# Kernel optimization log

Hardware: AMD Instinct MI355X
Metric: run time of the kernel (lower is better)

## Reference

```python
import jax, jax.numpy as jnp
import numpy as np

B, T, D, H = 2, 2048, 1024, 16
HS = D // H  # head_size = 64
EPS = 1e-5


def layer_norm(x, g, b):
    mu = jnp.mean(x, axis=-1, keepdims=True)
    var = jnp.var(x, axis=-1, keepdims=True)
    return (x - mu) * jax.lax.rsqrt(var + EPS) * g + b


def setup_inputs() -> dict:
    key = jax.random.key(0)
    ks = jax.random.split(key, 12)
    s_attn = 1.0 / np.sqrt(D)
    s_ff1 = 1.0 / np.sqrt(D)
    s_ff2 = 1.0 / np.sqrt(4 * D)
    return {
        "x": jax.random.normal(ks[0], (B, T, D), jnp.float32),
        "Wq": jax.random.normal(ks[1], (H, D, HS), jnp.float32) * s_attn,
        "Wk": jax.random.normal(ks[2], (H, D, HS), jnp.float32) * s_attn,
        "Wv": jax.random.normal(ks[3], (H, D, HS), jnp.float32) * s_attn,
        "Wo": jax.random.normal(ks[4], (H * HS, D), jnp.float32) * (1.0 / np.sqrt(H * HS)),
        "bo": jnp.zeros((D,), jnp.float32),
        "W1": jax.random.normal(ks[5], (D, 4 * D), jnp.float32) * s_ff1,
        "b1": jnp.zeros((4 * D,), jnp.float32),
        "W2": jax.random.normal(ks[6], (4 * D, D), jnp.float32) * s_ff2,
        "b2": jnp.zeros((D,), jnp.float32),
        "ln1_g": jnp.ones((D,), jnp.float32),
        "ln1_b": jnp.zeros((D,), jnp.float32),
        "ln2_g": jnp.ones((D,), jnp.float32),
        "ln2_b": jnp.zeros((D,), jnp.float32),
    }


def reference(x, Wq, Wk, Wv, Wo, bo, W1, b1, W2, b2, ln1_g, ln1_b, ln2_g, ln2_b):
    # --- self-attention on ln1(x) ---
    h = layer_norm(x, ln1_g, ln1_b)
    Q = jnp.einsum('bsd,hdk->bhsk', h, Wq)
    K = jnp.einsum('bsd,hdk->bhsk', h, Wk)
    V = jnp.einsum('bsd,hdk->bhsk', h, Wv)
    scores = jnp.einsum('bhqk,bhsk->bhqs', Q, K) * (HS ** -0.5)
    attn = jax.nn.softmax(scores, axis=-1)  # [B,H,T,T] non-causal, as in source
    out = jnp.einsum('bhqs,bhsk->bhqk', attn, V)
    out = out.transpose(0, 2, 1, 3).reshape(B, T, H * HS)  # concat heads
    sa = out @ Wo + bo
    x = x + sa
    # --- feed-forward on ln2(x) ---
    h2 = layer_norm(x, ln2_g, ln2_b)
    ff = jax.nn.relu(h2 @ W1 + b1) @ W2 + b2
    return x + ff
```

## Files before the change

### kernel.cpp

```cpp
#include <hip/hip_runtime.h>
#include <cstdint>
#include <cmath>

typedef __bf16 bf16;
typedef __bf16 bf16x8 __attribute__((ext_vector_type(8)));
typedef __bf16 bf16x4 __attribute__((ext_vector_type(4)));
typedef __bf16 bf16x2 __attribute__((ext_vector_type(2)));
typedef float  f32x4  __attribute__((ext_vector_type(4)));

#define B_   2
#define T_   2048
#define D_   1024
#define H_   16
#define HS_  64
#define NTOK (B_ * T_)

typedef __attribute__((address_space(1))) uint8_t* gp1_t;
typedef __attribute__((address_space(3))) uint8_t* lp3_t;
__device__ __forceinline__ void gl_lds16(const void* g, void* l) {
    __builtin_amdgcn_global_load_lds((gp1_t)(uintptr_t)g,
                                     (lp3_t)(uint32_t)(uintptr_t)l,
                                     16, 0, 0);
}

__device__ __forceinline__ f32x4 mfma16(bf16x8 a, bf16x8 b, f32x4 c) {
    return __builtin_amdgcn_mfma_f32_16x16x32_bf16(a, b, c, 0, 0, 0);
}

__device__ __forceinline__ uint32_t pk2(float lo, float hi) {
    uint32_t r;
    asm("v_cvt_pk_bf16_f32 %0, %1, %2" : "=v"(r) : "v"(lo), "v"(hi));
    return r;
}
__device__ __forceinline__ void pl32(uint32_t& a, uint32_t& b) {
    asm("v_permlane32_swap_b32 %0, %1" : "+v"(a), "+v"(b));
}
__device__ __forceinline__ void pl16(uint32_t& a, uint32_t& b) {
    asm("v_permlane16_swap_b32 %0, %1" : "+v"(a), "+v"(b));
}

__global__ __launch_bounds__(256) void prep_fused(
    const float* __restrict__ Wq, const float* __restrict__ Wk,
    const float* __restrict__ Wv, const float* __restrict__ Wo,
    const float* __restrict__ W1, const float* __restrict__ W2,
    const float* __restrict__ x,  const float* __restrict__ g,
    const float* __restrict__ be,
    bf16* __restrict__ WqkvT, bf16* __restrict__ WoT,
    bf16* __restrict__ W1T,  bf16* __restrict__ W2T,
    bf16* __restrict__ hbuf) {
    const int bid = blockIdx.x;
    const int tid = threadIdx.x;

    if (bid >= 12288) {
        const int row = bid - 12288;
        const float4 v = ((const float4*)(x + (size_t)row * 1024))[tid];
        float s  = v.x + v.y + v.z + v.w;
        float s2 = v.x * v.x + v.y * v.y + v.z * v.z + v.w * v.w;
        for (int m = 1; m < 64; m <<= 1) {
            s  += __shfl_xor(s, m);
            s2 += __shfl_xor(s2, m);
        }
        __shared__ float rs[4], rq[4];
        const int lane = tid & 63, wv = tid >> 6;
        if (lane == 0) { rs[wv] = s; rq[wv] = s2; }
        __syncthreads();
        s  = rs[0] + rs[1] + rs[2] + rs[3];
        s2 = rq[0] + rq[1] + rq[2] + rq[3];
        const float mu   = s * (1.f / 1024.f);
        const float var  = s2 * (1.f / 1024.f) - mu * mu;
        const float rstd = rsqrtf(var + 1e-5f);
        const float4 gg = ((const float4*)g)[tid];
        const float4 bb = ((const float4*)be)[tid];
        bf16x4 o;
        o[0] = (bf16)((v.x - mu) * rstd * gg.x + bb.x);
        o[1] = (bf16)((v.y - mu) * rstd * gg.y + bb.y);
        o[2] = (bf16)((v.z - mu) * rstd * gg.z + bb.z);
        o[3] = (bf16)((v.w - mu) * rstd * gg.w + bb.w);
        *(bf16x4*)(hbuf + (size_t)row * 1024 + tid * 4) = o;
        return;
    }

    const float* in; bf16* out;
    int C, R, bx, by;
    if (bid < 3072) {
        const int z = bid >> 6, rem = bid & 63;
        bx = rem & 1; by = rem >> 1;
        C = HS_; R = D_;
        in  = (z < 16 ? Wq : z < 32 ? Wk : Wv) + (size_t)(z & 15) * D_ * HS_;
        out = WqkvT + (size_t)z * HS_ * D_;
    } else if (bid < 4096) {
        const int rem = bid - 3072;
        bx = rem & 31; by = rem >> 5;
        C = 1024; R = 1024; in = Wo; out = WoT;
    } else if (bid < 8192) {
        const int rem = bid - 4096;
        bx = rem & 127; by = rem >> 7;
        C = 4096; R = 1024; in = W1; out = W1T;
    } else {
        const int rem = bid - 8192;
        bx = rem & 31; by = rem >> 5;
        C = 1024; R = 4096; in = W2; out = W2T;
    }
    const int tx = tid & 31, ty = tid >> 5;
    const int c0 = bx * 32, r0 = by * 32;
    __shared__ float t[32][33];
    for (int i = 0; i < 4; i++) {
        int r = ty + i * 8;
        t[r][tx] = in[(size_t)(r0 + r) * C + c0 + tx];
    }
    __syncthreads();
    for (int i = 0; i < 4; i++) {
        int rr = ty + i * 8;
        out[(size_t)(c0 + rr) * R + r0 + tx] = (bf16)t[tx][rr];
    }
}

__global__ __launch_bounds__(256) void ln_kernel(const float* __restrict__ x,
                                                 const float* __restrict__ g,
                                                 const float* __restrict__ b,
                                                 bf16* __restrict__ out) {
    const int row = blockIdx.x;
    const int tid = threadIdx.x;
    const float4 v = ((const float4*)(x + (size_t)row * 1024))[tid];
    float s  = v.x + v.y + v.z + v.w;
    float s2 = v.x * v.x + v.y * v.y + v.z * v.z + v.w * v.w;
    for (int m = 1; m < 64; m <<= 1) {
        s  += __shfl_xor(s, m);
        s2 += __shfl_xor(s2, m);
    }
    __shared__ float rs[4], rq[4];
    const int lane = tid & 63, wv = tid >> 6;
    if (lane == 0) { rs[wv] = s; rq[wv] = s2; }
    __syncthreads();
    s  = rs[0] + rs[1] + rs[2] + rs[3];
    s2 = rq[0] + rq[1] + rq[2] + rq[3];
    const float mu   = s * (1.f / 1024.f);
    const float var  = s2 * (1.f / 1024.f) - mu * mu;
    const float rstd = rsqrtf(var + 1e-5f);
    const float4 gg = ((const float4*)g)[tid];
    const float4 bb = ((const float4*)b)[tid];
    bf16x4 o;
    o[0] = (bf16)((v.x - mu) * rstd * gg.x + bb.x);
    o[1] = (bf16)((v.y - mu) * rstd * gg.y + bb.y);
    o[2] = (bf16)((v.z - mu) * rstd * gg.z + bb.z);
    o[3] = (bf16)((v.w - mu) * rstd * gg.w + bb.w);
    *(bf16x4*)(out + (size_t)row * 1024 + tid * 4) = o;
}

__global__ __launch_bounds__(256) void combine4(const float* __restrict__ p0,
                                                const float* __restrict__ p1,
                                                const float* __restrict__ p2,
                                                const float* __restrict__ p3,
                                                const float* __restrict__ resid,
                                                const float* __restrict__ bias,
                                                float* __restrict__ out) {
    const int i4 = blockIdx.x * 256 + threadIdx.x;
    const float4 a = ((const float4*)p0)[i4];
    const float4 b = ((const float4*)p1)[i4];
    const float4 c = ((const float4*)p2)[i4];
    const float4 d = ((const float4*)p3)[i4];
    const float4 r = ((const float4*)resid)[i4];
    const float4 bb = ((const float4*)bias)[i4 & 255];
    float4 o;
    o.x = a.x + b.x + c.x + d.x + r.x + bb.x;
    o.y = a.y + b.y + c.y + d.y + r.y + bb.y;
    o.z = a.z + b.z + c.z + d.z + r.z + bb.z;
    o.w = a.w + b.w + c.w + d.w + r.w + bb.w;
    ((float4*)out)[i4] = o;
}

template <int BIAS, int RELU, int RES, int OUTBF16, int VTP = 0>
__global__ __launch_bounds__(256, 2) void gemm_bt(
    const bf16* __restrict__ A, const bf16* __restrict__ Bt,
    const float* __restrict__ bias, const float* __restrict__ resid,
    void* __restrict__ Cout, bf16* __restrict__ Vt, int M, int N, int K) {
    __shared__ __align__(16) bf16 As[2][128 * 32];
    __shared__ __align__(16) bf16 Bs[2][128 * 32];
    const int tid  = threadIdx.x;
    const int lane = tid & 63, w = tid >> 6;
    const int quad = lane >> 4, l15 = lane & 15;
    const int m0 = blockIdx.y * 128, n0 = blockIdx.x * 128;
    const int wm = (w & 1) * 64, wn = (w >> 1) * 64;

    f32x4 acc[4][4];
    for (int i = 0; i < 4; i++)
        for (int j = 0; j < 4; j++) acc[i][j] = f32x4{0.f, 0.f, 0.f, 0.f};

    const int arow = lane >> 2;
    const int acol = (lane & 3) * 8;
    const int c0 = w * 2, c1 = w * 2 + 1;

    for (int kt = 0; kt < K; kt += 64) {
        gl_lds16(A  + (size_t)(m0 + c0 * 16 + arow) * K + kt + acol,      &As[0][c0 * 512]);
        gl_lds16(A  + (size_t)(m0 + c1 * 16 + arow) * K + kt + acol,      &As[0][c1 * 512]);
        gl_lds16(A  + (size_t)(m0 + c0 * 16 + arow) * K + kt + 32 + acol, &As[1][c0 * 512]);
        gl_lds16(A  + (size_t)(m0 + c1 * 16 + arow) * K + kt + 32 + acol, &As[1][c1 * 512]);
        gl_lds16(Bt + (size_t)(n0 + c0 * 16 + arow) * K + kt + acol,      &Bs[0][c0 * 512]);
        gl_lds16(Bt + (size_t)(n0 + c1 * 16 + arow) * K + kt + acol,      &Bs[0][c1 * 512]);
        gl_lds16(Bt + (size_t)(n0 + c0 * 16 + arow) * K + kt + 32 + acol, &Bs[1][c0 * 512]);
        gl_lds16(Bt + (size_t)(n0 + c1 * 16 + arow) * K + kt + 32 + acol, &Bs[1][c1 * 512]);
        __syncthreads();
        for (int kh = 0; kh < 2; kh++) {
            bf16x8 af[4], bfr[4];
            for (int mi = 0; mi < 4; mi++)
                af[mi] = *(const bf16x8*)&As[kh][(wm + mi * 16 + l15) * 32 + quad * 8];
            for (int ni = 0; ni < 4; ni++)
                bfr[ni] = *(const bf16x8*)&Bs[kh][(wn + ni * 16 + l15) * 32 + quad * 8];
            for (int mi = 0; mi < 4; mi++)
                for (int ni = 0; ni < 4; ni++)
                    acc[mi][ni] = mfma16(af[mi], bfr[ni], acc[mi][ni]);
        }
        __syncthreads();
    }

    for (int mi = 0; mi < 4; mi++) {
        for (int ni = 0; ni < 4; ni++) {
            const int colb = n0 + wn + ni * 16 + l15;
            if (VTP && colb >= 2048) {
                const int h = (colb - 2048) >> 6, hs = (colb - 2048) & 63;
                const int row0 = m0 + wm + mi * 16 + quad * 4;
                const int b = row0 >> 11;
                bf16x4 p4;
                p4[0] = (bf16)acc[mi][ni][0];
                p4[1] = (bf16)acc[mi][ni][1];
                p4[2] = (bf16)acc[mi][ni][2];
                p4[3] = (bf16)acc[mi][ni][3];
                *(bf16x4*)&Vt[((size_t)(b * 16 + h) * 64 + hs) * T_ + (row0 & 2047)] = p4;
                continue;
            }
            const float bv = BIAS ? bias[colb] : 0.f;
            for (int r = 0; r < 4; r++) {
                const int row = m0 + wm + mi * 16 + quad * 4 + r;
                float v = acc[mi][ni][r] + bv;
                if (RELU) v = fmaxf(v, 0.f);
                if (RES)  v += resid[(size_t)row * N + colb];
                if (OUTBF16) ((bf16*)Cout)[(size_t)row * N + colb] = (bf16)v;
                else         ((float*)Cout)[(size_t)row * N + colb] = v;
            }
        }
    }
}

template <int BIAS, int RELU, int VTP, int PARTIAL>
__global__ __launch_bounds__(512, 2) void gemm256(
    const bf16* __restrict__ A, const bf16* __restrict__ Bt,
    const float* __restrict__ bias, void* __restrict__ Cout,
    bf16* __restrict__ Vt, float* __restrict__ P0, float* __restrict__ P1,
    int M, int N, int K) {
    __shared__ __align__(16) bf16 Asub[4][256 * 32];
    __shared__ __align__(16) bf16 Bsub[4][256 * 32];
    const int tid  = threadIdx.x;
    const int lane = tid & 63, w = tid >> 6;
    const int wr = w >> 2, wc = w & 3;
    const int quad = lane >> 4, l15 = lane & 15;
    const int m0 = blockIdx.y * 256, n0 = blockIdx.x * 256;
    const int kpb = PARTIAL ? (K / (int)gridDim.z) : K;
    const int k0  = PARTIAL ? (int)blockIdx.z * kpb : 0;
    const int S   = kpb / 32;

    const int slog = (((lane & 3) ^ ((lane >> 3) & 3)) * 8);
    const int crow = lane >> 2;
    const bf16* gA0 = A  + (size_t)(m0 + 32 * w + crow)      * K + k0 + slog;
    const bf16* gA1 = A  + (size_t)(m0 + 32 * w + 16 + crow) * K + k0 + slog;
    const bf16* gB0 = Bt + (size_t)(n0 + 32 * w + crow)      * K + k0 + slog;
    const bf16* gB1 = Bt + (size_t)(n0 + 32 * w + 16 + crow) * K + k0 + slog;

    for (int t = 0; t < 3; t++) {
        gl_lds16(gA0, &Asub[t][(32 * w) * 32]);
        gl_lds16(gA1, &Asub[t][(32 * w + 16) * 32]);
        gl_lds16(gB0, &Bsub[t][(32 * w) * 32]);
        gl_lds16(gB1, &Bsub[t][(32 * w + 16) * 32]);
        gA0 += 32; gA1 += 32; gB0 += 32; gB1 += 32;
    }

    f32x4 acc[8][4];
#pragma unroll
    for (int i = 0; i < 8; i++)
#pragma unroll
        for (int j = 0; j < 4; j++) acc[i][j] = f32x4{0.f, 0.f, 0.f, 0.f};

    const int swz = (quad ^ ((l15 >> 1) & 3)) * 8;
    const int aof = (wr * 128 + l15) * 32 + swz;
    const int bof = (wc * 64 + l15) * 32 + swz;

    asm volatile("s_waitcnt vmcnt(8)" ::: "memory");
    __builtin_amdgcn_sched_barrier(0);
    __builtin_amdgcn_s_barrier();

    for (int s = 0; s < S; s++) {
        const bf16* Ab = &Asub[s & 3][0];
        const bf16* Bb = &Bsub[s & 3][0];
        const int pb = (s + 3) & 3;
        bf16x8 af[4], bfr[4];
#pragma unroll
        for (int f = 0; f < 4; f++) af[f] = *(const bf16x8*)&Ab[aof + f * 512];
#pragma unroll
        for (int n = 0; n < 4; n++) bfr[n] = *(const bf16x8*)&Bb[bof + n * 512];
        if (s + 3 < S) {
            gl_lds16(gA0, &Asub[pb][(32 * w) * 32]);
            gl_lds16(gA1, &Asub[pb][(32 * w + 16) * 32]);
            gA0 += 32; gA1 += 32;
        }
        asm volatile("s_waitcnt lgkmcnt(0)" ::: "memory");
        __builtin_amdgcn_sched_barrier(0);
        __builtin_amdgcn_s_setprio(1);
#pragma unroll
        for (int f = 0; f < 4; f++)
#pragma unroll
            for (int n = 0; n < 4; n++)
                acc[f][n] = mfma16(af[f], bfr[n], acc[f][n]);
        __builtin_amdgcn_s_setprio(0);
#pragma unroll
        for (int f = 0; f < 4; f++) af[f] = *(const bf16x8*)&Ab[aof + 2048 + f * 512];
        if (s + 3 < S) {
            gl_lds16(gB0, &Bsub[pb][(32 * w) * 32]);
            gl_lds16(gB1, &Bsub[pb][(32 * w + 16) * 32]);
            gB0 += 32; gB1 += 32;
        }
        asm volatile("s_waitcnt lgkmcnt(0)" ::: "memory");
        __builtin_amdgcn_sched_barrier(0);
        __builtin_amdgcn_s_setprio(1);
#pragma unroll
        for (int f = 0; f < 4; f++)
#pragma unroll
            for (int n = 0; n < 4; n++)
                acc[4 + f][n] = mfma16(af[f], bfr[n], acc[4 + f][n]);
        __builtin_amdgcn_s_setprio(0);
        __builtin_amdgcn_sched_barrier(0);
        if (s <= S - 4)      asm volatile("s_waitcnt vmcnt(8)" ::: "memory");
        else if (s == S - 3) asm volatile("s_waitcnt vmcnt(4)" ::: "memory");
        else if (s == S - 2) asm volatile("s_waitcnt vmcnt(0)" ::: "memory");
        __builtin_amdgcn_s_barrier();
    }

#pragma unroll
    for (int mi = 0; mi < 8; mi++) {
#pragma unroll
        for (int ni = 0; ni < 4; ni++) {
            const int colb = n0 + wc * 64 + ni * 16 + l15;
            const int row0 = m0 + wr * 128 + (mi >> 2) * 64 + (mi & 3) * 16 + quad * 4;
            if (VTP && colb >= 2048) {
                const int h = (colb - 2048) >> 6, hs = (colb - 2048) & 63;
                const int b = row0 >> 11;
                bf16x4 p4;
                p4[0] = (bf16)acc[mi][ni][0];
                p4[1] = (bf16)acc[mi][ni][1];
                p4[2] = (bf16)acc[mi][ni][2];
                p4[3] = (bf16)acc[mi][ni][3];
                *(bf16x4*)&Vt[((size_t)(b * 16 + h) * 64 + hs) * T_ + (row0 & 2047)] = p4;
                continue;
            }
            if (PARTIAL) {
                float* Cz = ((int)blockIdx.z < 2 ? P0 : P1) + (size_t)(blockIdx.z & 1) * M * N;
                for (int r = 0; r < 4; r++)
                    Cz[(size_t)(row0 + r) * N + colb] = acc[mi][ni][r];
            } else {
                const float bv = BIAS ? bias[colb] : 0.f;
                for (int r = 0; r < 4; r++) {
                    float v = acc[mi][ni][r] + bv;
                    if (RELU) v = fmaxf(v, 0.f);
                    ((bf16*)Cout)[(size_t)(row0 + r) * N + colb] = (bf16)v;
                }
            }
        }
    }
}

#define LSTR 68
#define NJ   (T_ / 64)
__global__ __launch_bounds__(256, 2) void flash_attn(const bf16* __restrict__ QKV,
                                                     const bf16* __restrict__ Vt,
                                                     bf16* __restrict__ attn_out) {
    const int bh = blockIdx.y, b = bh >> 4, h = bh & 15;
    const int q0 = blockIdx.x * 128;
    const int tid = threadIdx.x, lane = tid & 63, w = tid >> 6;
    const int quad = lane >> 4, l15 = lane & 15;
    __shared__ __align__(16) bf16 Ks[2][64 * LSTR];
    __shared__ __align__(16) bf16 Vs[2][64 * LSTR];
    const bf16* Qb = QKV + (size_t)b * T_ * 3072 + h * 64;
    const bf16* Kb = QKV + (size_t)b * T_ * 3072 + 1024 + h * 64;
    const bf16* Vb = Vt  + (size_t)bh * HS_ * T_;

    const float sc = 0.125f * 1.44269504088896f;
    const int sr = tid >> 2, scc = (tid & 3) * 16;

    bf16x8 QA[2][2];
    for (int qnt = 0; qnt < 2; qnt++) {
        const size_t row = (size_t)(q0 + w * 32 + qnt * 16 + l15) * 3072;
        for (int kk = 0; kk < 2; kk++) {
            bf16x8 q = *(const bf16x8*)&Qb[row + kk * 32 + quad * 8];
            for (int i = 0; i < 8; i++) q[i] = (bf16)((float)q[i] * sc);
            QA[qnt][kk] = q;
        }
    }

    bf16x8 ones8;
    for (int i = 0; i < 8; i++) ones8[i] = (bf16)1.0f;

    f32x4 O[2][4], lacc[2];
    for (int mi = 0; mi < 2; mi++) {
        lacc[mi] = f32x4{0.f, 0.f, 0.f, 0.f};
        for (int n = 0; n < 4; n++) O[mi][n] = f32x4{0.f, 0.f, 0.f, 0.f};
    }

    *(bf16x8*)&Ks[0][sr * LSTR + scc]     = *(const bf16x8*)&Kb[(size_t)sr * 3072 + scc];
    *(bf16x8*)&Ks[0][sr * LSTR + scc + 8] = *(const bf16x8*)&Kb[(size_t)sr * 3072 + scc + 8];
    *(bf16x8*)&Vs[0][sr * LSTR + scc]     = *(const bf16x8*)&Vb[(size_t)sr * T_ + scc];
    *(bf16x8*)&Vs[0][sr * LSTR + scc + 8] = *(const bf16x8*)&Vb[(size_t)sr * T_ + scc + 8];
    __syncthreads();

    bf16x8 k0, k1, v0, v1;
    for (int j = 0; j < NJ; j++) {
        const int buf = j & 1;
        if (j + 1 < NJ) {
            const int s1 = (j + 1) * 64;
            k0 = *(const bf16x8*)&Kb[(size_t)(s1 + sr) * 3072 + scc];
            k1 = *(const bf16x8*)&Kb[(size_t)(s1 + sr) * 3072 + scc + 8];
            v0 = *(const bf16x8*)&Vb[(size_t)sr * T_ + s1 + scc];
            v1 = *(const bf16x8*)&Vb[(size_t)sr * T_ + s1 + scc + 8];
        }
        bf16x8 KB[4][2];
#pragma unroll
        for (int smt = 0; smt < 4; smt++)
#pragma unroll
            for (int kk = 0; kk < 2; kk++)
                KB[smt][kk] = *(const bf16x8*)&Ks[buf][(smt * 16 + l15) * LSTR + kk * 32 + quad * 8];

        bf16x8 PA[2][2];
#pragma unroll
        for (int qnt = 0; qnt < 2; qnt++) {
            f32x4 ST[4];
#pragma unroll
            for (int smt = 0; smt < 4; smt++) ST[smt] = f32x4{0.f, 0.f, 0.f, 0.f};
            __builtin_amdgcn_s_setprio(1);
#pragma unroll
            for (int kk = 0; kk < 2; kk++)
#pragma unroll
                for (int smt = 0; smt < 4; smt++)
                    ST[smt] = mfma16(KB[smt][kk], QA[qnt][kk], ST[smt]);
            __builtin_amdgcn_s_setprio(0);
            uint32_t w00 = pk2(__builtin_amdgcn_exp2f(ST[0][0]), __builtin_amdgcn_exp2f(ST[0][1]));
            uint32_t w01 = pk2(__builtin_amdgcn_exp2f(ST[0][2]), __builtin_amdgcn_exp2f(ST[0][3]));
            uint32_t w10 = pk2(__builtin_amdgcn_exp2f(ST[1][0]), __builtin_amdgcn_exp2f(ST[1][1]));
            uint32_t w11 = pk2(__builtin_amdgcn_exp2f(ST[1][2]), __builtin_amdgcn_exp2f(ST[1][3]));
            uint32_t w20 = pk2(__builtin_amdgcn_exp2f(ST[2][0]), __builtin_amdgcn_exp2f(ST[2][1]));
            uint32_t w21 = pk2(__builtin_amdgcn_exp2f(ST[2][2]), __builtin_amdgcn_exp2f(ST[2][3]));
            uint32_t w30 = pk2(__builtin_amdgcn_exp2f(ST[3][0]), __builtin_amdgcn_exp2f(ST[3][1]));
            uint32_t w31 = pk2(__builtin_amdgcn_exp2f(ST[3][2]), __builtin_amdgcn_exp2f(ST[3][3]));
            pl32(w00, w10); pl16(w00, w10);
            pl32(w01, w11); pl16(w01, w11);
            pl32(w20, w30); pl16(w20, w30);
            pl32(w21, w31); pl16(w21, w31);
            union { uint32_t u[4]; bf16x8 v; } pa0, pa1;
            pa0.u[0] = w00; pa0.u[1] = w01; pa0.u[2] = w10; pa0.u[3] = w11;
            pa1.u[0] = w20; pa1.u[1] = w21; pa1.u[2] = w30; pa1.u[3] = w31;
            PA[qnt][0] = pa0.v;
            PA[qnt][1] = pa1.v;
        }
        bf16x8 VB[4][2];
#pragma unroll
        for (int n = 0; n < 4; n++)
#pragma unroll
            for (int kk = 0; kk < 2; kk++)
                VB[n][kk] = *(const bf16x8*)&Vs[buf][(n * 16 + l15) * LSTR + kk * 32 + quad * 8];
        __builtin_amdgcn_s_setprio(1);
#pragma unroll
        for (int mi = 0; mi < 2; mi++) {
            const bf16x8 PA0 = PA[mi][0];
            const bf16x8 PA1 = PA[mi][1];
#pragma unroll
            for (int n = 0; n < 4; n++) {
                O[mi][n] = mfma16(PA0, VB[n][0], O[mi][n]);
                O[mi][n] = mfma16(PA1, VB[n][1], O[mi][n]);
            }
            lacc[mi] = mfma16(PA0, ones8, lacc[mi]);
            lacc[mi] = mfma16(PA1, ones8, lacc[mi]);
        }
        __builtin_amdgcn_s_setprio(0);
        if (j + 1 < NJ) {
            *(bf16x8*)&Ks[buf ^ 1][sr * LSTR + scc]     = k0;
            *(bf16x8*)&Ks[buf ^ 1][sr * LSTR + scc + 8] = k1;
            *(bf16x8*)&Vs[buf ^ 1][sr * LSTR + scc]     = v0;
            *(bf16x8*)&Vs[buf ^ 1][sr * LSTR + scc + 8] = v1;
        }
        __syncthreads();
    }

    for (int mi = 0; mi < 2; mi++) {
        for (int r = 0; r < 4; r++) {
            const float inv = 1.f / lacc[mi][r];
            const size_t tok = (size_t)b * T_ + q0 + w * 32 + mi * 16 + quad * 4 + r;
            for (int n = 0; n < 4; n++)
                attn_out[tok * 1024 + h * 64 + n * 16 + l15] = (bf16)(O[mi][n][r] * inv);
        }
    }
}

extern "C" void kernel_launch(void* const* d_in, const int* in_sizes, int n_in,
                              void* d_out, int out_size, void* d_ws, size_t ws_size,
                              hipStream_t stream) {
    const float* x   = (const float*)d_in[0];
    const float* Wq  = (const float*)d_in[1];
    const float* Wk  = (const float*)d_in[2];
    const float* Wv  = (const float*)d_in[3];
    const float* Wo  = (const float*)d_in[4];
    const float* bo  = (const float*)d_in[5];
    const float* W1  = (const float*)d_in[6];
    const float* b1  = (const float*)d_in[7];
    const float* W2  = (const float*)d_in[8];
    const float* b2  = (const float*)d_in[9];
    const float* g1  = (const float*)d_in[10];
    const float* be1 = (const float*)d_in[11];
    const float* g2  = (const float*)d_in[12];
    const float* be2 = (const float*)d_in[13];

    char* ws = (char*)d_ws;
    const size_t MB = 1ull << 20;
    bf16*  WqkvT = (bf16*)(ws);
    bf16*  WoT   = (bf16*)(ws + 6  * MB);
    bf16*  W1T   = (bf16*)(ws + 8  * MB);
    bf16*  W2T   = (bf16*)(ws + 16 * MB);
    bf16*  hbuf  = (bf16*)(ws + 24 * MB);
    bf16*  QKV   = (bf16*)(ws + 32 * MB);
    bf16*  Vt    = (bf16*)(ws + 56 * MB);
    bf16*  attn  = (bf16*)(ws + 64 * MB);
    float* x2    = (float*)(ws + 72 * MB);
    bf16*  ff1   = (bf16*)(ws + 32 * MB);
    float* partA = (float*)(ws);
    float* partB = (float*)(ws + 88 * MB);
    float* out   = (float*)d_out;

    prep_fused<<<16384, 256, 0, stream>>>(Wq, Wk, Wv, Wo, W1, W2, x, g1, be1,
                                          WqkvT, WoT, W1T, W2T, hbuf);
    gemm_bt<0, 0, 0, 1, 1><<<dim3(24, 32), 256, 0, stream>>>(
        hbuf, WqkvT, nullptr, nullptr, QKV, Vt, NTOK, 3072, 1024);
    flash_attn<<<dim3(T_ / 128, B_ * H_), 256, 0, stream>>>(QKV, Vt, attn);
    gemm_bt<1, 0, 1, 0><<<dim3(8, 32), 256, 0, stream>>>(
        attn, WoT, bo, x, x2, nullptr, NTOK, 1024, 1024);
    ln_kernel<<<NTOK, 256, 0, stream>>>(x2, g2, be2, hbuf);
    gemm256<1, 1, 0, 0><<<dim3(16, 16), 512, 0, stream>>>(
        hbuf, W1T, b1, ff1, nullptr, nullptr, nullptr, NTOK, 4096, 1024);
    gemm256<0, 0, 0, 1><<<dim3(4, 16, 4), 512, 0, stream>>>(
        ff1, W2T, nullptr, nullptr, nullptr, partA, partB, NTOK, 1024, 4096);
    combine4<<<NTOK, 256, 0, stream>>>(partA, partA + (size_t)NTOK * 1024,
                                       partB, partB + (size_t)NTOK * 1024,
                                       x2, b2, out);
}
```

Before: 331.1 us.

## Pipeline 128-tile GEMM with 4-stage LDS ring and drop split-K for FFN2

```diff
diff --git a/kernel.cpp b/kernel.cpp
--- a/kernel.cpp
+++ b/kernel.cpp
@@ -147,70 +147,79 @@
     *(bf16x4*)(out + (size_t)row * 1024 + tid * 4) = o;
 }
 
-__global__ __launch_bounds__(256) void combine4(const float* __restrict__ p0,
-                                                const float* __restrict__ p1,
-                                                const float* __restrict__ p2,
-                                                const float* __restrict__ p3,
-                                                const float* __restrict__ resid,
-                                                const float* __restrict__ bias,
-                                                float* __restrict__ out) {
-    const int i4 = blockIdx.x * 256 + threadIdx.x;
-    const float4 a = ((const float4*)p0)[i4];
-    const float4 b = ((const float4*)p1)[i4];
-    const float4 c = ((const float4*)p2)[i4];
-    const float4 d = ((const float4*)p3)[i4];
-    const float4 r = ((const float4*)resid)[i4];
-    const float4 bb = ((const float4*)bias)[i4 & 255];
-    float4 o;
-    o.x = a.x + b.x + c.x + d.x + r.x + bb.x;
-    o.y = a.y + b.y + c.y + d.y + r.y + bb.y;
-    o.z = a.z + b.z + c.z + d.z + r.z + bb.z;
-    o.w = a.w + b.w + c.w + d.w + r.w + bb.w;
-    ((float4*)out)[i4] = o;
-}
-
 template <int BIAS, int RELU, int RES, int OUTBF16, int VTP = 0>
-__global__ __launch_bounds__(256, 2) void gemm_bt(
+__global__ __launch_bounds__(256, 2) void gemm128v2(
     const bf16* __restrict__ A, const bf16* __restrict__ Bt,
     const float* __restrict__ bias, const float* __restrict__ resid,
     void* __restrict__ Cout, bf16* __restrict__ Vt, int M, int N, int K) {
-    __shared__ __align__(16) bf16 As[2][128 * 32];
-    __shared__ __align__(16) bf16 Bs[2][128 * 32];
+    __shared__ __align__(16) bf16 Asub[4][128 * 32];
+    __shared__ __align__(16) bf16 Bsub[4][128 * 32];
     const int tid  = threadIdx.x;
     const int lane = tid & 63, w = tid >> 6;
     const int quad = lane >> 4, l15 = lane & 15;
     const int m0 = blockIdx.y * 128, n0 = blockIdx.x * 128;
     const int wm = (w & 1) * 64, wn = (w >> 1) * 64;
+    const int S  = K / 32;
+
+    const int slog = (((lane & 3) ^ ((lane >> 3) & 3)) * 8);
+    const int crow = lane >> 2;
+    const bf16* gA0 = A  + (size_t)(m0 + 32 * w + crow)      * K + slog;
+    const bf16* gA1 = A  + (size_t)(m0 + 32 * w + 16 + crow) * K + slog;
+    const bf16* gB0 = Bt + (size_t)(n0 + 32 * w + crow)      * K + slog;
+    const bf16* gB1 = Bt + (size_t)(n0 + 32 * w + 16 + crow) * K + slog;
+
+    for (int t = 0; t < 3; t++) {
+        gl_lds16(gA0, &Asub[t][(32 * w) * 32]);
+        gl_lds16(gA1, &Asub[t][(32 * w + 16) * 32]);
+        gl_lds16(gB0, &Bsub[t][(32 * w) * 32]);
+        gl_lds16(gB1, &Bsub[t][(32 * w + 16) * 32]);
+        gA0 += 32; gA1 += 32; gB0 += 32; gB1 += 32;
+    }
 
     f32x4 acc[4][4];
+#pragma unroll
     for (int i = 0; i < 4; i++)
+#pragma unroll
         for (int j = 0; j < 4; j++) acc[i][j] = f32x4{0.f, 0.f, 0.f, 0.f};
 
-    const int arow = lane >> 2;
-    const int acol = (lane & 3) * 8;
-    const int c0 = w * 2, c1 = w * 2 + 1;
-
-    for (int kt = 0; kt < K; kt += 64) {
-        gl_lds16(A  + (size_t)(m0 + c0 * 16 + arow) * K + kt + acol,      &As[0][c0 * 512]);
-        gl_lds16(A  + (size_t)(m0 + c1 * 16 + arow) * K + kt + acol,      &As[0][c1 * 512]);
-        gl_lds16(A  + (size_t)(m0 + c0 * 16 + arow) * K + kt + 32 + acol, &As[1][c0 * 512]);
-        gl_lds16(A  + (size_t)(m0 + c1 * 16 + arow) * K + kt + 32 + acol, &As[1][c1 * 512]);
-        gl_lds16(Bt + (size_t)(n0 + c0 * 16 + arow) * K + kt + acol,      &Bs[0][c0 * 512]);
-        gl_lds16(Bt + (size_t)(n0 + c1 * 16 + arow) * K + kt + acol,      &Bs[0][c1 * 512]);
-        gl_lds16(Bt + (size_t)(n0 + c0 * 16 + arow) * K + kt + 32 + acol, &Bs[1][c0 * 512]);
-        gl_lds16(Bt + (size_t)(n0 + c1 * 16 + arow) * K + kt + 32 + acol, &Bs[1][c1 * 512]);
-        __syncthreads();
-        for (int kh = 0; kh < 2; kh++) {
-            bf16x8 af[4], bfr[4];
-            for (int mi = 0; mi < 4; mi++)
-                af[mi] = *(const bf16x8*)&As[kh][(wm + mi * 16 + l15) * 32 + quad * 8];
+    const int swz = (quad ^ ((l15 >> 1) & 3)) * 8;
+    const int aof = (wm + l15) * 32 + swz;
+    const int bof = (wn + l15) * 32 + swz;
+
+    asm volatile("s_waitcnt vmcnt(8)" ::: "memory");
+    __builtin_amdgcn_sched_barrier(0);
+    __builtin_amdgcn_s_barrier();
+
+    for (int s = 0; s < S; s++) {
+        const bf16* Ab = &Asub[s & 3][0];
+        const bf16* Bb = &Bsub[s & 3][0];
+        const int pb = (s + 3) & 3;
+        bf16x8 af[4], bfr[4];
+#pragma unroll
+        for (int mi = 0; mi < 4; mi++) af[mi] = *(const bf16x8*)&Ab[aof + mi * 512];
+#pragma unroll
+        for (int ni = 0; ni < 4; ni++) bfr[ni] = *(const bf16x8*)&Bb[bof + ni * 512];
+        if (s + 3 < S) {
+            gl_lds16(gA0, &Asub[pb][(32 * w) * 32]);
+            gl_lds16(gA1, &Asub[pb][(32 * w + 16) * 32]);
+            gl_lds16(gB0, &Bsub[pb][(32 * w) * 32]);
+            gl_lds16(gB1, &Bsub[pb][(32 * w + 16) * 32]);
+            gA0 += 32; gA1 += 32; gB0 += 32; gB1 += 32;
+        }
+        asm volatile("s_waitcnt lgkmcnt(0)" ::: "memory");
+        __builtin_amdgcn_sched_barrier(0);
+        __builtin_amdgcn_s_setprio(1);
+#pragma unroll
+        for (int mi = 0; mi < 4; mi++)
+#pragma unroll
             for (int ni = 0; ni < 4; ni++)
-                bfr[ni] = *(const bf16x8*)&Bs[kh][(wn + ni * 16 + l15) * 32 + quad * 8];
-            for (int mi = 0; mi < 4; mi++)
-                for (int ni = 0; ni < 4; ni++)
-                    acc[mi][ni] = mfma16(af[mi], bfr[ni], acc[mi][ni]);
-        }
-        __syncthreads();
+                acc[mi][ni] = mfma16(af[mi], bfr[ni], acc[mi][ni]);
+        __builtin_amdgcn_s_setprio(0);
+        __builtin_amdgcn_sched_barrier(0);
+        if (s <= S - 4)      asm volatile("s_waitcnt vmcnt(8)" ::: "memory");
+        else if (s == S - 3) asm volatile("s_waitcnt vmcnt(4)" ::: "memory");
+        else if (s == S - 2) asm volatile("s_waitcnt vmcnt(0)" ::: "memory");
+        __builtin_amdgcn_s_barrier();
     }
 
     for (int mi = 0; mi < 4; mi++) {
@@ -241,11 +250,10 @@
     }
 }
 
-template <int BIAS, int RELU, int VTP, int PARTIAL>
+template <int BIAS, int RELU>
 __global__ __launch_bounds__(512, 2) void gemm256(
     const bf16* __restrict__ A, const bf16* __restrict__ Bt,
     const float* __restrict__ bias, void* __restrict__ Cout,
-    bf16* __restrict__ Vt, float* __restrict__ P0, float* __restrict__ P1,
     int M, int N, int K) {
     __shared__ __align__(16) bf16 Asub[4][256 * 32];
     __shared__ __align__(16) bf16 Bsub[4][256 * 32];
@@ -254,16 +262,14 @@
     const int wr = w >> 2, wc = w & 3;
     const int quad = lane >> 4, l15 = lane & 15;
     const int m0 = blockIdx.y * 256, n0 = blockIdx.x * 256;
-    const int kpb = PARTIAL ? (K / (int)gridDim.z) : K;
-    const int k0  = PARTIAL ? (int)blockIdx.z * kpb : 0;
-    const int S   = kpb / 32;
+    const int S   = K / 32;
 
     const int slog = (((lane & 3) ^ ((lane >> 3) & 3)) * 8);
     const int crow = lane >> 2;
-    const bf16* gA0 = A  + (size_t)(m0 + 32 * w + crow)      * K + k0 + slog;
-    const bf16* gA1 = A  + (size_t)(m0 + 32 * w + 16 + crow) * K + k0 + slog;
-    const bf16* gB0 = Bt + (size_t)(n0 + 32 * w + crow)      * K + k0 + slog;
-    const bf16* gB1 = Bt + (size_t)(n0 + 32 * w + 16 + crow) * K + k0 + slog;
+    const bf16* gA0 = A  + (size_t)(m0 + 32 * w + crow)      * K + slog;
+    const bf16* gA1 = A  + (size_t)(m0 + 32 * w + 16 + crow) * K + slog;
+    const bf16* gB0 = Bt + (size_t)(n0 + 32 * w + crow)      * K + slog;
+    const bf16* gB1 = Bt + (size_t)(n0 + 32 * w + 16 + crow) * K + slog;
 
     for (int t = 0; t < 3; t++) {
         gl_lds16(gA0, &Asub[t][(32 * w) * 32]);
@@ -339,28 +345,11 @@
         for (int ni = 0; ni < 4; ni++) {
             const int colb = n0 + wc * 64 + ni * 16 + l15;
             const int row0 = m0 + wr * 128 + (mi >> 2) * 64 + (mi & 3) * 16 + quad * 4;
-            if (VTP && colb >= 2048) {
-                const int h = (colb - 2048) >> 6, hs = (colb - 2048) & 63;
-                const int b = row0 >> 11;
-                bf16x4 p4;
-                p4[0] = (bf16)acc[mi][ni][0];
-                p4[1] = (bf16)acc[mi][ni][1];
-                p4[2] = (bf16)acc[mi][ni][2];
-                p4[3] = (bf16)acc[mi][ni][3];
-                *(bf16x4*)&Vt[((size_t)(b * 16 + h) * 64 + hs) * T_ + (row0 & 2047)] = p4;
-                continue;
-            }
-            if (PARTIAL) {
-                float* Cz = ((int)blockIdx.z < 2 ? P0 : P1) + (size_t)(blockIdx.z & 1) * M * N;
-                for (int r = 0; r < 4; r++)
-                    Cz[(size_t)(row0 + r) * N + colb] = acc[mi][ni][r];
-            } else {
-                const float bv = BIAS ? bias[colb] : 0.f;
-                for (int r = 0; r < 4; r++) {
-                    float v = acc[mi][ni][r] + bv;
-                    if (RELU) v = fmaxf(v, 0.f);
-                    ((bf16*)Cout)[(size_t)(row0 + r) * N + colb] = (bf16)v;
-                }
+            const float bv = BIAS ? bias[colb] : 0.f;
+            for (int r = 0; r < 4; r++) {
+                float v = acc[mi][ni][r] + bv;
+                if (RELU) v = fmaxf(v, 0.f);
+                ((bf16*)Cout)[(size_t)(row0 + r) * N + colb] = (bf16)v;
             }
         }
     }
@@ -526,23 +515,18 @@
     bf16*  attn  = (bf16*)(ws + 64 * MB);
     float* x2    = (float*)(ws + 72 * MB);
     bf16*  ff1   = (bf16*)(ws + 32 * MB);
-    float* partA = (float*)(ws);
-    float* partB = (float*)(ws + 88 * MB);
     float* out   = (float*)d_out;
 
     prep_fused<<<16384, 256, 0, stream>>>(Wq, Wk, Wv, Wo, W1, W2, x, g1, be1,
                                           WqkvT, WoT, W1T, W2T, hbuf);
-    gemm_bt<0, 0, 0, 1, 1><<<dim3(24, 32), 256, 0, stream>>>(
+    gemm128v2<0, 0, 0, 1, 1><<<dim3(24, 32), 256, 0, stream>>>(
         hbuf, WqkvT, nullptr, nullptr, QKV, Vt, NTOK, 3072, 1024);
     flash_attn<<<dim3(T_ / 128, B_ * H_), 256, 0, stream>>>(QKV, Vt, attn);
-    gemm_bt<1, 0, 1, 0><<<dim3(8, 32), 256, 0, stream>>>(
+    gemm128v2<1, 0, 1, 0><<<dim3(8, 32), 256, 0, stream>>>(
         attn, WoT, bo, x, x2, nullptr, NTOK, 1024, 1024);
     ln_kernel<<<NTOK, 256, 0, stream>>>(x2, g2, be2, hbuf);
-    gemm256<1, 1, 0, 0><<<dim3(16, 16), 512, 0, stream>>>(
-        hbuf, W1T, b1, ff1, nullptr, nullptr, nullptr, NTOK, 4096, 1024);
-    gemm256<0, 0, 0, 1><<<dim3(4, 16, 4), 512, 0, stream>>>(
-        ff1, W2T, nullptr, nullptr, nullptr, partA, partB, NTOK, 1024, 4096);
-    combine4<<<NTOK, 256, 0, stream>>>(partA, partA + (size_t)NTOK * 1024,
-                                       partB, partB + (size_t)NTOK * 1024,
-                                       x2, b2, out);
-}
+    gemm256<1, 1><<<dim3(16, 16), 512, 0, stream>>>(
+        hbuf, W1T, b1, ff1, NTOK, 4096, 1024);
+    gemm128v2<1, 0, 1, 0><<<dim3(8, 32), 256, 0, stream>>>(
+        ff1, W2T, b2, x2, out, nullptr, NTOK, 1024, 4096);
+}
```

Result: faster. 313.6 us (-5.3%).
